# Kernel optimization log

Hardware: AMD Instinct MI355X
Metric: run time of the kernel (lower is better)

## Reference

```python
import jax, jax.numpy as jnp
import numpy as np

D_KEY, BANK_N = 128, 9720
BS, N = 1, 1620          # n = h*w = 30*54 (480p features, stride 16)
D_VAL, C, OBJ_N = 512, 512, 3


def setup_inputs() -> dict:
    key = jax.random.key(0)
    k1, k2, k3, k4, k5 = jax.random.split(key, 5)
    return {
        "keys_bank": jax.random.normal(k1, (D_KEY, BANK_N), dtype=jnp.float32),
        "q_in": jax.random.normal(k2, (BS, D_KEY, N), dtype=jnp.float32),
        "q_out": jax.random.normal(k3, (OBJ_N, C, N), dtype=jnp.float32),
        "values": jax.random.normal(k4, (OBJ_N, D_VAL, BANK_N), dtype=jnp.float32),
        "masks": jax.random.uniform(k5, (OBJ_N, 1, BANK_N), dtype=jnp.float32),
    }


def reference(keys_bank, q_in, q_out, values, masks):
    # p[b,k,n] = softmax_k( keys^T q_in / sqrt(d_key) )
    d_key = keys_bank.shape[0]
    scale = 1.0 / np.sqrt(d_key).astype(np.float32)
    p = jnp.einsum("dk,bdn->bkn", keys_bank, q_in) * scale
    p = jax.nn.softmax(p, axis=1)  # over bank dim

    # Batched over objects (original loops per object, sharing p)
    mem = jnp.einsum("ovk,bkn->obvn", values, p)       # (obj, bs, d_val, n)
    mask_mem = jnp.einsum("ouk,bkn->obun", masks, p)   # (obj, bs, 1, n)
    q_out_with_mask = q_out[:, None, :, :] * mask_mem  # (obj, bs, C, n)

    out = jnp.concatenate([mem, q_out_with_mask], axis=2)  # (obj, bs, d_val+C, n)
    return jnp.swapaxes(out, 0, 1)                          # (bs, obj, d_val+C, n)
```

## Files before the change

kernel.cpp:

```cpp
#include <hip/hip_runtime.h>
#include <hip/hip_bf16.h>

typedef unsigned short u16;
typedef unsigned char  u8;

#define D_KEY   128
#define BANK_N  9720
#define BANK_P  9728
#define N_TOK   1620
#define N_PAD   1664
#define OBJ_N   3
#define M_PAD   1664
#define LDCOL   1664
#define ONES_ROW 1539
#define QK_SCALE 0.08838834764831845f
#define KITERS  76
#define QK_BLOCKS 988

typedef __bf16 bf16x8 __attribute__((ext_vector_type(8)));
typedef float  f32x4  __attribute__((ext_vector_type(4)));
typedef unsigned int u32x4 __attribute__((ext_vector_type(4)));
typedef int i32x8 __attribute__((ext_vector_type(8)));

__device__ __forceinline__ float bf2f(u16 u) {
  union { unsigned int i; float f; } v; v.i = ((unsigned int)u) << 16; return v.f;
}
__device__ __forceinline__ u16 f2bf(float f) {
  unsigned int x = __float_as_uint(f);
  unsigned int r = x + 0x7fffu + ((x >> 16) & 1u);
  return (u16)(r >> 16);
}
__device__ __forceinline__ unsigned pack_fp8x4(float a, float b, float c, float d) {
  unsigned v = __builtin_amdgcn_cvt_pk_fp8_f32(a, b, 0, false);
  v = __builtin_amdgcn_cvt_pk_fp8_f32(c, d, v, true);
  return v;
}
__device__ __forceinline__ u8 f2fp8(float a) {
  return (u8)(__builtin_amdgcn_cvt_pk_fp8_f32(a, 0.f, 0, false) & 0xff);
}

__device__ __forceinline__ void load_lds16(const void* g, void* l) {
  __builtin_amdgcn_global_load_lds(
      (const __attribute__((address_space(1))) void*)g,
      (__attribute__((address_space(3))) void*)l, 16, 0, 0);
}

__global__ void prep(const float* __restrict__ q, const float* __restrict__ keys,
                     u16* __restrict__ qT, u16* __restrict__ kT) {
  __shared__ float t[64][65];
  int b = blockIdx.x;
  const int tx = threadIdx.x & 63;
  const int ty = threadIdx.x >> 6;
  if (b < 52) {
    const int bd = (b & 1) * 64;
    const int bn = (b >> 1) * 64;
#pragma unroll
    for (int i = 0; i < 64; i += 4) {
      int d = bd + ty + i;
      int n = bn + tx;
      t[ty + i][tx] = (n < N_TOK) ? q[(size_t)d * N_TOK + n] : 0.f;
    }
    __syncthreads();
#pragma unroll
    for (int i = 0; i < 64; i += 4) {
      int r = ty + i;
      qT[(size_t)(bn + r) * D_KEY + bd + tx] = f2bf(t[tx][r] * QK_SCALE);
    }
    return;
  }
  b -= 52;
  const int bk = (b % 152) * 64;
  const int bd = (b / 152) * 64;
#pragma unroll
  for (int i = 0; i < 64; i += 4) {
    int d = bd + ty + i;
    int k = bk + tx;
    t[ty + i][tx] = (k < BANK_N) ? keys[(size_t)d * BANK_N + k] : 0.f;
  }
  __syncthreads();
#pragma unroll
  for (int i = 0; i < 64; i += 4) {
    int r = ty + i;
    kT[(size_t)(bk + r) * D_KEY + bd + tx] = f2bf(t[tx][r]);
  }
}

__global__ void gemm_qk_vm(const u16* __restrict__ A, const u16* __restrict__ B,
                           u8* __restrict__ E8,
                           const float* __restrict__ values,
                           const float* __restrict__ masks,
                           u8* __restrict__ vm8)
{
  __shared__ __align__(16) u16 sbuf[8192];

  if (blockIdx.x >= QK_BLOCKS) {
    const int NV = BANK_P / 16;
    int idx = (blockIdx.x - QK_BLOCKS) * 256 + threadIdx.x;
    if (idx >= M_PAD * NV) return;
    int m = idx / NV;
    int k16 = (idx - m * NV) * 16;
    const bool ones = (m == ONES_ROW);
    const float* src = nullptr;
    if (m < 1536)          src = values + (size_t)m * BANK_N;
    else if (m < ONES_ROW) src = masks + (size_t)(m - 1536) * BANK_N;
    u32x4 outv;
#pragma unroll
    for (int c = 0; c < 4; c++) {
      int k4 = k16 + c * 4;
      float4 v = make_float4(0.f, 0.f, 0.f, 0.f);
      if (ones) {
        v.x = (k4     < BANK_N) ? 1.f : 0.f;
        v.y = (k4 + 1 < BANK_N) ? 1.f : 0.f;
        v.z = (k4 + 2 < BANK_N) ? 1.f : 0.f;
        v.w = (k4 + 3 < BANK_N) ? 1.f : 0.f;
      } else if (src) {
        if (k4 + 3 < BANK_N) v = *(const float4*)(src + k4);
        else {
          if (k4     < BANK_N) v.x = src[k4];
          if (k4 + 1 < BANK_N) v.y = src[k4 + 1];
          if (k4 + 2 < BANK_N) v.z = src[k4 + 2];
          if (k4 + 3 < BANK_N) v.w = src[k4 + 3];
        }
      }
      outv[c] = pack_fp8x4(v.x, v.y, v.z, v.w);
    }
    *(u32x4*)(vm8 + (size_t)m * BANK_P + k16) = outv;
    return;
  }

  u16* As = sbuf;
  u16* Bs = sbuf + 4096;

  const int tid  = threadIdx.x;
  const int wave = tid >> 6;
  const int lane = tid & 63;
  const int bn = blockIdx.x % 76, bm = blockIdx.x / 76;

  const u16* Abase = A + (size_t)bm * 128 * D_KEY;
  const u16* Bbase = B + (size_t)bn * 128 * D_KEY;

  const int r  = lane >> 2;
  const int c8 = (lane & 3) << 3;
  const int s0 = wave, s1 = wave + 4;

  f32x4 acc[4][4];
#pragma unroll
  for (int i = 0; i < 4; i++)
#pragma unroll
    for (int j = 0; j < 4; j++) acc[i][j] = (f32x4){0.f, 0.f, 0.f, 0.f};

  const int m_in = lane & 15;
  const int quad = lane >> 4;
  const int wm = (wave >> 1) * 64;
  const int wn = (wave & 1) * 64;

  for (int kt = 0; kt < D_KEY; kt += 32) {
    load_lds16(Abase + (size_t)(s0 * 16 + r) * D_KEY + kt + c8, &As[s0 * 512]);
    load_lds16(Abase + (size_t)(s1 * 16 + r) * D_KEY + kt + c8, &As[s1 * 512]);
    load_lds16(Bbase + (size_t)(s0 * 16 + r) * D_KEY + kt + c8, &Bs[s0 * 512]);
    load_lds16(Bbase + (size_t)(s1 * 16 + r) * D_KEY + kt + c8, &Bs[s1 * 512]);
    __syncthreads();

    bf16x8 af[4], bfr[4];
#pragma unroll
    for (int i = 0; i < 4; i++)
      af[i] = *(const bf16x8*)&As[(wm + i * 16 + m_in) * 32 + quad * 8];
#pragma unroll
    for (int j = 0; j < 4; j++)
      bfr[j] = *(const bf16x8*)&Bs[(wn + j * 16 + m_in) * 32 + quad * 8];
#pragma unroll
    for (int i = 0; i < 4; i++)
#pragma unroll
      for (int j = 0; j < 4; j++)
        acc[i][j] = __builtin_amdgcn_mfma_f32_16x16x32_bf16(af[i], bfr[j], acc[i][j], 0, 0, 0);
    __syncthreads();
  }

  u8* sb8 = (u8*)sbuf;
#pragma unroll
  for (int i = 0; i < 4; i++)
#pragma unroll
    for (int j = 0; j < 4; j++)
#pragma unroll
      for (int t = 0; t < 4; t++) {
        int row_l = wm + i * 16 + quad * 4 + t;
        int col_l = wn + j * 16 + m_in;
        bool valid = (bn * 128 + col_l) < BANK_N;
        sb8[(row_l << 7) + col_l] = valid ? f2fp8(__expf(acc[i][j][t])) : (u8)0;
      }
  __syncthreads();

  for (int chunk = tid; chunk < 1024; chunk += 256) {
    int row = chunk >> 3;
    int cu  = (chunk & 7) << 4;
    u32x4 v = *(const u32x4*)&sb8[(row << 7) + cu];
    *(u32x4*)&E8[(size_t)(bm * 128 + row) * BANK_P + bn * 128 + cu] = v;
  }
}

__global__ __launch_bounds__(256, 2)
void gemm_pv(const u8* __restrict__ A, const u8* __restrict__ B,
             u16* __restrict__ memC, int nParts, size_t cPartStride)
{
  __shared__ __align__(16) u16 sbuf[32768];
  u8* const lds0 = (u8*)sbuf;

  const int tid  = threadIdx.x;
  const int wave = tid >> 6;
  const int lane = tid & 63;

  const int bq = (int)gridDim.x >> 3, br = (int)gridDim.x & 7;
  const int xcd = blockIdx.x & 7, bj = blockIdx.x >> 3;
  int b = (xcd < br ? xcd * (bq + 1) : br * (bq + 1) + (xcd - br) * bq) + bj;

  int bz = b / 169;
  int rr = b - bz * 169;
  int gid = rr / 52;
  int rem = rr - gid * 52;
  int width = (gid < 3) ? 4 : 1;
  int bm = rem / width;
  int bn = gid * 4 + (rem - bm * width);

  const int base = KITERS / nParts;
  const int remP = KITERS - base * nParts;
  const int nt    = base + (bz < remP ? 1 : 0);
  const int itbeg = bz * base + (bz < remP ? bz : remP);
  const int kbeg  = itbeg * 128;

  const u8* Abase = A + (size_t)bm * 128 * BANK_P;
  const u8* Bbase = B + (size_t)bn * 128 * BANK_P;

  const int srow  = lane >> 1;
  const int shalf = (((lane & 1) ^ ((lane >> 3) & 1)) << 4);
  const size_t arow_off = (size_t)(wave * 32 + srow) * BANK_P;

  f32x4 acc[4][4];
#pragma unroll
  for (int i = 0; i < 4; i++)
#pragma unroll
    for (int j = 0; j < 4; j++) acc[i][j] = (f32x4){0.f, 0.f, 0.f, 0.f};

  const int m_in = lane & 15;
  const int quad = lane >> 4;
  const int wm = (wave >> 1) * 64;
  const int wn = (wave & 1) * 64;
  const int fxor = ((m_in >> 2) & 1) << 4;

  auto stage = [&](int tile, int q) {
    const int kt = kbeg + tile * 128;
    u8* dst = lds0 + q * 32768;
#pragma unroll
    for (int s = 0; s < 4; s++)
      load_lds16(Abase + arow_off + kt + s * 32 + shalf, dst + s * 4096 + wave * 1024);
#pragma unroll
    for (int s = 0; s < 4; s++)
      load_lds16(Bbase + arow_off + kt + s * 32 + shalf, dst + 16384 + s * 4096 + wave * 1024);
  };

  stage(0, 0);
  stage(1, 1);
  asm volatile("s_waitcnt vmcnt(8)" ::: "memory");
  __builtin_amdgcn_s_barrier();
  __builtin_amdgcn_sched_barrier(0);

  for (int t = 0; t < nt; ++t) {
    const u8* As8 = lds0 + (t & 1) * 32768;
    const u8* Bs8 = As8 + 16384;

    __builtin_amdgcn_s_setprio(1);
    i32x8 a8[4];
#pragma unroll
    for (int i = 0; i < 4; i++) {
      const u8* p = As8 + quad * 4096 + (wm + i * 16 + m_in) * 32;
      u32x4 lo = *(const u32x4*)(p + fxor);
      u32x4 hi = *(const u32x4*)(p + (fxor ^ 16));
      a8[i] = (i32x8){(int)lo[0], (int)lo[1], (int)lo[2], (int)lo[3],
                      (int)hi[0], (int)hi[1], (int)hi[2], (int)hi[3]};
    }
#pragma unroll
    for (int j = 0; j < 4; j++) {
      const u8* p = Bs8 + quad * 4096 + (wn + j * 16 + m_in) * 32;
      u32x4 lo = *(const u32x4*)(p + fxor);
      u32x4 hi = *(const u32x4*)(p + (fxor ^ 16));
      i32x8 b8 = (i32x8){(int)lo[0], (int)lo[1], (int)lo[2], (int)lo[3],
                         (int)hi[0], (int)hi[1], (int)hi[2], (int)hi[3]};
#pragma unroll
      for (int i = 0; i < 4; i++)
        acc[i][j] = __builtin_amdgcn_mfma_scale_f32_16x16x128_f8f6f4(
            a8[i], b8, acc[i][j], 0, 0,
            0, 0x7f7f7f7f, 0, 0x7f7f7f7f);
    }
    __builtin_amdgcn_s_setprio(0);

    if (t + 1 >= nt) break;

    __builtin_amdgcn_sched_barrier(0);
    __builtin_amdgcn_s_barrier();
    if (t + 2 < nt) {
      stage(t + 2, t & 1);
      asm volatile("s_waitcnt vmcnt(8)" ::: "memory");
    } else {
      asm volatile("s_waitcnt vmcnt(0)" ::: "memory");
    }
    __builtin_amdgcn_s_barrier();
    __builtin_amdgcn_sched_barrier(0);
  }

  __syncthreads();

  u16* Cg = memC + (size_t)bz * cPartStride;
#pragma unroll
  for (int h = 0; h < 2; h++) {
    __syncthreads();
    if ((wave >> 1) == h) {
#pragma unroll
      for (int i = 0; i < 4; i++)
#pragma unroll
        for (int j = 0; j < 4; j++)
#pragma unroll
          for (int t = 0; t < 4; t++) {
            int row_l = i * 16 + quad * 4 + t;
            int col_l = wn + j * 16 + m_in;
            sbuf[(row_l << 7) + col_l] = f2bf(acc[i][j][t]);
          }
    }
    __syncthreads();
    for (int chunk = tid; chunk < 1024; chunk += 256) {
      int row = chunk >> 4;
      int cu  = (chunk & 15) << 3;
      u32x4 v = *(const u32x4*)&sbuf[(row << 7) + cu];
      *(u32x4*)&Cg[(size_t)(bm * 128 + h * 64 + row) * LDCOL + bn * 128 + cu] = v;
    }
  }
}

__global__ void epilogue(const u16* __restrict__ memC, const float* __restrict__ q_out,
                         float* __restrict__ out, int nParts) {
  const int NV = N_TOK / 4;
  int idx = blockIdx.x * 256 + threadIdx.x;
  if (idx >= OBJ_N * 1024 * NV) return;
  int n4 = (idx % NV) * 4;
  int t = idx / NV;
  int c = t & 1023;
  int o = t >> 10;
  const size_t ps = (size_t)M_PAD * LDCOL;

  const u16* lbase = memC + (size_t)ONES_ROW * LDCOL + n4;
  float4 l = make_float4(0.f, 0.f, 0.f, 0.f);
  for (int z = 0; z < nParts; z++) {
    ushort4 v = *(const ushort4*)(lbase + z * ps);
    l.x += bf2f(v.x); l.y += bf2f(v.y); l.z += bf2f(v.z); l.w += bf2f(v.w);
  }

  size_t rowoff = (c < 512) ? (size_t)(o * 512 + c) * LDCOL
                            : (size_t)(1536 + o) * LDCOL;
  const u16* base = memC + rowoff + n4;
  float4 s = make_float4(0.f, 0.f, 0.f, 0.f);
  for (int z = 0; z < nParts; z++) {
    ushort4 v = *(const ushort4*)(base + z * ps);
    s.x += bf2f(v.x); s.y += bf2f(v.y); s.z += bf2f(v.z); s.w += bf2f(v.w);
  }
  float4 rv;
  float ix = 1.f / l.x, iy = 1.f / l.y, iz = 1.f / l.z, iw = 1.f / l.w;
  if (c < 512) {
    rv.x = s.x * ix; rv.y = s.y * iy; rv.z = s.z * iz; rv.w = s.w * iw;
  } else {
    float4 q = *(const float4*)(q_out + (size_t)(o * 512 + (c - 512)) * N_TOK + n4);
    rv.x = q.x * s.x * ix; rv.y = q.y * s.y * iy;
    rv.z = q.z * s.z * iz; rv.w = q.w * s.w * iw;
  }
  *(float4*)(out + (size_t)(o * 1024 + c) * N_TOK + n4) = rv;
}

extern "C" void kernel_launch(void* const* d_in, const int* in_sizes, int n_in,
                              void* d_out, int out_size, void* d_ws, size_t ws_size,
                              hipStream_t stream) {
  const float* keys   = (const float*)d_in[0];
  const float* q_in   = (const float*)d_in[1];
  const float* q_out  = (const float*)d_in[2];
  const float* values = (const float*)d_in[3];
  const float* masks  = (const float*)d_in[4];
  float* out = (float*)d_out;

  char* ws = (char*)d_ws;
  size_t off = 0;
  auto alloc = [&](size_t bytes) -> void* {
    void* p = ws + off; off += (bytes + 255) & ~(size_t)255; return p;
  };
  u16* qT  = (u16*)alloc((size_t)N_PAD * D_KEY * 2);
  u16* kT  = (u16*)alloc((size_t)BANK_P * D_KEY * 2);
  u8*  vm8 = (u8*)alloc((size_t)M_PAD * BANK_P);
  u8*  E8  = (u8*)alloc((size_t)N_PAD * BANK_P);

  int nParts = 8;
  while (nParts > 1 && off + (size_t)nParts * M_PAD * LDCOL * 2 > ws_size) nParts >>= 1;
  u16* memC = (u16*)alloc((size_t)nParts * M_PAD * LDCOL * 2);

  prep<<<356, 256, 0, stream>>>(q_in, keys, qT, kT);

  const int vmBlocks = (M_PAD * (BANK_P / 16) + 255) / 256;
  gemm_qk_vm<<<QK_BLOCKS + vmBlocks, 256, 0, stream>>>(qT, kT, E8, values, masks, vm8);

  gemm_pv<<<dim3(169 * nParts), 256, 0, stream>>>(vm8, E8, memC, nParts, (size_t)M_PAD * LDCOL);

  epilogue<<<(OBJ_N * 1024 * (N_TOK / 4) + 255) / 256, 256, 0, stream>>>(
      memC, q_out, out, nParts);
}
```

Measured before the change: 194.0 us.

## Switch PV GEMM to 32x32x64 FP8 MFMA with smaller k-tiles

```diff
diff --git a/kernel.cpp b/kernel.cpp
--- a/kernel.cpp
+++ b/kernel.cpp
@@ -19,6 +19,7 @@
 
 typedef __bf16 bf16x8 __attribute__((ext_vector_type(8)));
 typedef float  f32x4  __attribute__((ext_vector_type(4)));
+typedef float  f32x16 __attribute__((ext_vector_type(16)));
 typedef unsigned int u32x4 __attribute__((ext_vector_type(4)));
 typedef int i32x8 __attribute__((ext_vector_type(8)));
 
@@ -198,11 +199,11 @@
   }
 }
 
-__global__ __launch_bounds__(256, 2)
+__global__ __launch_bounds__(256, 4)
 void gemm_pv(const u8* __restrict__ A, const u8* __restrict__ B,
              u16* __restrict__ memC, int nParts, size_t cPartStride)
 {
-  __shared__ __align__(16) u16 sbuf[32768];
+  __shared__ __align__(16) u16 sbuf[16384];
   u8* const lds0 = (u8*)sbuf;
 
   const int tid  = threadIdx.x;
@@ -223,82 +224,92 @@
 
   const int base = KITERS / nParts;
   const int remP = KITERS - base * nParts;
-  const int nt    = base + (bz < remP ? 1 : 0);
+  const int nt128 = base + (bz < remP ? 1 : 0);
   const int itbeg = bz * base + (bz < remP ? bz : remP);
   const int kbeg  = itbeg * 128;
+  const int kN    = nt128 * 2;
 
   const u8* Abase = A + (size_t)bm * 128 * BANK_P;
   const u8* Bbase = B + (size_t)bn * 128 * BANK_P;
 
-  const int srow  = lane >> 1;
-  const int shalf = (((lane & 1) ^ ((lane >> 3) & 1)) << 4);
-  const size_t arow_off = (size_t)(wave * 32 + srow) * BANK_P;
-
-  f32x4 acc[4][4];
-#pragma unroll
-  for (int i = 0; i < 4; i++)
-#pragma unroll
-    for (int j = 0; j < 4; j++) acc[i][j] = (f32x4){0.f, 0.f, 0.f, 0.f};
-
-  const int m_in = lane & 15;
-  const int quad = lane >> 4;
-  const int wm = (wave >> 1) * 64;
-  const int wn = (wave & 1) * 64;
-  const int fxor = ((m_in >> 2) & 1) << 4;
-
-  auto stage = [&](int tile, int q) {
-    const int kt = kbeg + tile * 128;
-    u8* dst = lds0 + q * 32768;
-#pragma unroll
-    for (int s = 0; s < 4; s++)
-      load_lds16(Abase + arow_off + kt + s * 32 + shalf, dst + s * 4096 + wave * 1024);
-#pragma unroll
-    for (int s = 0; s < 4; s++)
-      load_lds16(Bbase + arow_off + kt + s * 32 + shalf, dst + 16384 + s * 4096 + wave * 1024);
+  f32x16 acc[2][2];
+#pragma unroll
+  for (int i = 0; i < 2; i++)
+#pragma unroll
+    for (int j = 0; j < 2; j++)
+#pragma unroll
+      for (int r = 0; r < 16; r++) acc[i][j][r] = 0.f;
+
+  const int l31  = lane & 31;
+  const int h    = lane >> 5;
+  const int wm   = (wave >> 1) * 64;
+  const int wn   = (wave & 1) * 64;
+
+  const int srow0 = wave * 32 + (lane >> 2);
+  const int sswz0 = ((lane & 3) ^ ((srow0 >> 1) & 3)) << 4;
+  const int srow1 = srow0 + 16;
+  const int sswz1 = ((lane & 3) ^ ((srow1 >> 1) & 3)) << 4;
+  const size_t soffA0 = (size_t)srow0 * BANK_P + sswz0;
+  const size_t soffA1 = (size_t)srow1 * BANK_P + sswz1;
+
+  auto stage = [&](int t64, int q) {
+    const int kt = kbeg + t64 * 64;
+    u8* dst = lds0 + q * 16384 + wave * 2048;
+    load_lds16(Abase + soffA0 + kt, dst);
+    load_lds16(Abase + soffA1 + kt, dst + 1024);
+    load_lds16(Bbase + soffA0 + kt, dst + 8192);
+    load_lds16(Bbase + soffA1 + kt, dst + 8192 + 1024);
   };
+
 
   stage(0, 0);
   stage(1, 1);
-  asm volatile("s_waitcnt vmcnt(8)" ::: "memory");
+  asm volatile("s_waitcnt vmcnt(4)" ::: "memory");
   __builtin_amdgcn_s_barrier();
   __builtin_amdgcn_sched_barrier(0);
 
-  for (int t = 0; t < nt; ++t) {
-    const u8* As8 = lds0 + (t & 1) * 32768;
-    const u8* Bs8 = As8 + 16384;
+  for (int t = 0; t < kN; ++t) {
+    const u8* As8 = lds0 + (t & 1) * 16384;
+    const u8* Bs8 = As8 + 8192;
 
     __builtin_amdgcn_s_setprio(1);
-    i32x8 a8[4];
-#pragma unroll
-    for (int i = 0; i < 4; i++) {
-      const u8* p = As8 + quad * 4096 + (wm + i * 16 + m_in) * 32;
-      u32x4 lo = *(const u32x4*)(p + fxor);
-      u32x4 hi = *(const u32x4*)(p + (fxor ^ 16));
-      a8[i] = (i32x8){(int)lo[0], (int)lo[1], (int)lo[2], (int)lo[3],
+    i32x8 a8[2], b8[2];
+#pragma unroll
+    for (int m = 0; m < 2; m++) {
+      const int row = wm + m * 32 + l31;
+      const int s = (row >> 1) & 3;
+      const u8* p = As8 + row * 64;
+      u32x4 lo = *(const u32x4*)(p + (((2 * h)     ^ s) << 4));
+      u32x4 hi = *(const u32x4*)(p + (((2 * h + 1) ^ s) << 4));
+      a8[m] = (i32x8){(int)lo[0], (int)lo[1], (int)lo[2], (int)lo[3],
                       (int)hi[0], (int)hi[1], (int)hi[2], (int)hi[3]};
     }
 #pragma unroll
-    for (int j = 0; j < 4; j++) {
-      const u8* p = Bs8 + quad * 4096 + (wn + j * 16 + m_in) * 32;
-      u32x4 lo = *(const u32x4*)(p + fxor);
-      u32x4 hi = *(const u32x4*)(p + (fxor ^ 16));
-      i32x8 b8 = (i32x8){(int)lo[0], (int)lo[1], (int)lo[2], (int)lo[3],
-                         (int)hi[0], (int)hi[1], (int)hi[2], (int)hi[3]};
-#pragma unroll
-      for (int i = 0; i < 4; i++)
-        acc[i][j] = __builtin_amdgcn_mfma_scale_f32_16x16x128_f8f6f4(
-            a8[i], b8, acc[i][j], 0, 0,
+    for (int n = 0; n < 2; n++) {
+      const int row = wn + n * 32 + l31;
+      const int s = (row >> 1) & 3;
+      const u8* p = Bs8 + row * 64;
+      u32x4 lo = *(const u32x4*)(p + (((2 * h)     ^ s) << 4));
+      u32x4 hi = *(const u32x4*)(p + (((2 * h + 1) ^ s) << 4));
+      b8[n] = (i32x8){(int)lo[0], (int)lo[1], (int)lo[2], (int)lo[3],
+                      (int)hi[0], (int)hi[1], (int)hi[2], (int)hi[3]};
+    }
+#pragma unroll
+    for (int n = 0; n < 2; n++)
+#pragma unroll
+      for (int m = 0; m < 2; m++)
+        acc[m][n] = __builtin_amdgcn_mfma_scale_f32_32x32x64_f8f6f4(
+            a8[m], b8[n], acc[m][n], 0, 0,
             0, 0x7f7f7f7f, 0, 0x7f7f7f7f);
-    }
     __builtin_amdgcn_s_setprio(0);
 
-    if (t + 1 >= nt) break;
+    if (t + 1 >= kN) break;
 
     __builtin_amdgcn_sched_barrier(0);
     __builtin_amdgcn_s_barrier();
-    if (t + 2 < nt) {
+    if (t + 2 < kN) {
       stage(t + 2, t & 1);
-      asm volatile("s_waitcnt vmcnt(8)" ::: "memory");
+      asm volatile("s_waitcnt vmcnt(4)" ::: "memory");
     } else {
       asm volatile("s_waitcnt vmcnt(0)" ::: "memory");
     }
@@ -310,18 +321,18 @@
 
   u16* Cg = memC + (size_t)bz * cPartStride;
 #pragma unroll
-  for (int h = 0; h < 2; h++) {
+  for (int hh = 0; hh < 2; hh++) {
     __syncthreads();
-    if ((wave >> 1) == h) {
-#pragma unroll
-      for (int i = 0; i < 4; i++)
-#pragma unroll
-        for (int j = 0; j < 4; j++)
-#pragma unroll
-          for (int t = 0; t < 4; t++) {
-            int row_l = i * 16 + quad * 4 + t;
-            int col_l = wn + j * 16 + m_in;
-            sbuf[(row_l << 7) + col_l] = f2bf(acc[i][j][t]);
+    if ((wave >> 1) == hh) {
+#pragma unroll
+      for (int m = 0; m < 2; m++)
+#pragma unroll
+        for (int n = 0; n < 2; n++)
+#pragma unroll
+          for (int r = 0; r < 16; r++) {
+            int row_l = m * 32 + (r & 3) + 8 * (r >> 2) + 4 * h;
+            int col_l = (wave & 1) * 64 + n * 32 + l31;
+            sbuf[(row_l << 7) + col_l] = f2bf(acc[m][n][r]);
           }
     }
     __syncthreads();
@@ -329,7 +340,7 @@
       int row = chunk >> 4;
       int cu  = (chunk & 15) << 3;
       u32x4 v = *(const u32x4*)&sbuf[(row << 7) + cu];
-      *(u32x4*)&Cg[(size_t)(bm * 128 + h * 64 + row) * LDCOL + bn * 128 + cu] = v;
+      *(u32x4*)&Cg[(size_t)(bm * 128 + hh * 64 + row) * LDCOL + bn * 128 + cu] = v;
     }
   }
 }
```

Result: faster. 189.0 us (-2.6%).
